# Performance work log

Measured on AMD Instinct MI355X. Metric: run time of the kernel, lower is better.

The kernel has to match this reference:

```python
import jax, jax.numpy as jnp
import numpy as np

N_NODES = 50000
N_EDGES = 800000
HID = 128
LAYERS = 3


def setup_inputs() -> dict:
    key = jax.random.key(0)
    k1, k2, k3, k4 = jax.random.split(key, 4)
    x = jax.random.normal(k1, (N_NODES, HID), dtype=jnp.float32)
    edge_index = jax.random.randint(k2, (2, N_EDGES), 0, N_NODES, dtype=jnp.int64)
    # Glorot-ish scale so 3 stacked layers stay numerically tame
    Ws = jax.random.normal(k3, (LAYERS, HID, HID), dtype=jnp.float32) * (1.0 / np.sqrt(HID))
    bs = jax.random.normal(k4, (LAYERS, HID), dtype=jnp.float32) * 0.01
    return {"x": x, "edge_index": edge_index, "Ws": Ws, "bs": bs}


def reference(x, edge_index, Ws, bs):
    """Stacked GCNConv (add_self_loops=False): out = D^-1/2 A D^-1/2 (x W) + b.
    Returns (final_x, embeddings_list) like the torch module."""
    N = x.shape[0]
    src = edge_index[0]  # message sources (x_j)
    dst = edge_index[1]  # aggregation targets
    # gcn_norm with unit edge weights, no self loops: in-degree on targets
    deg = jax.ops.segment_sum(jnp.ones(src.shape[0], dtype=x.dtype), dst, num_segments=N)
    dinv = jnp.where(deg > 0, jax.lax.rsqrt(jnp.maximum(deg, 1.0)), 0.0).astype(x.dtype)
    norm = dinv[src] * dinv[dst]  # [E]

    embeddings = [x]
    for l in range(Ws.shape[0]):
        h = x @ Ws[l]                               # [N, D] dense transform
        msg = h[src] * norm[:, None]                # [E, D] gather + normalize
        x = jax.ops.segment_sum(msg, dst, num_segments=N) + bs[l]  # scatter-add
        embeddings.append(x)
    return (x, embeddings)
```

## Files before the change

kernel.cpp:

```cpp
#include <hip/hip_runtime.h>

#define N_NODES 50000
#define N_EDGES 800000
#define HID 128
#define SLOT (N_NODES * HID)
#define W_STRIDE (HID * HID)

#define OFF_CNT    0ul
#define OFF_DINV   200192ul
#define OFF_RPTR   400384ul
#define OFF_RFILL  600576ul
#define OFF_BSUM   800768ul
#define OFF_BOFS   801280ul
#define OFF_SRCS   801792ul
#define OFF_H_WS   4001792ul


__global__ void k_zero_cnt(int* __restrict__ cnt) {
    int i = blockIdx.x * blockDim.x + threadIdx.x;
    if (i < N_NODES) cnt[i] = 0;
}

__global__ void k_count(const int* __restrict__ ei, int* __restrict__ cnt) {
    int e = blockIdx.x * blockDim.x + threadIdx.x;
    if (e < N_EDGES) {
        int d = ei[N_EDGES + e];
        atomicAdd(&cnt[d], 1);
    }
}

__global__ void k_dinv(const int* __restrict__ cnt, float* __restrict__ dinv) {
    int i = blockIdx.x * blockDim.x + threadIdx.x;
    if (i < N_NODES) {
        int c = cnt[i];
        dinv[i] = (c > 0) ? rsqrtf((float)c) : 0.0f;
    }
}

__global__ void k_scan_block(const int* __restrict__ cnt, int* __restrict__ rptr,
                             int* __restrict__ bsum) {
    __shared__ int s[512];
    int tid = threadIdx.x;
    int gid = blockIdx.x * 512 + tid;
    int v = (gid < N_NODES) ? cnt[gid] : 0;
    s[tid] = v;
    __syncthreads();
    for (int off = 1; off < 512; off <<= 1) {
        int t = (tid >= off) ? s[tid - off] : 0;
        __syncthreads();
        s[tid] += t;
        __syncthreads();
    }
    if (gid < N_NODES) rptr[gid] = s[tid] - v;
    if (tid == 511) bsum[blockIdx.x] = s[511];
}

__global__ void k_scan_sums(const int* __restrict__ bsum, int* __restrict__ bofs, int nb) {
    __shared__ int s[128];
    int tid = threadIdx.x;
    int v = (tid < nb) ? bsum[tid] : 0;
    s[tid] = v;
    __syncthreads();
    for (int off = 1; off < 128; off <<= 1) {
        int t = (tid >= off) ? s[tid - off] : 0;
        __syncthreads();
        s[tid] += t;
        __syncthreads();
    }
    if (tid < nb) bofs[tid] = s[tid] - v;
}

__global__ void k_scan_add(int* __restrict__ rptr, int* __restrict__ rfill,
                           const int* __restrict__ bofs) {
    int gid = blockIdx.x * blockDim.x + threadIdx.x;
    if (gid < N_NODES) {
        int r = rptr[gid] + bofs[gid >> 9];
        rptr[gid] = r;
        rfill[gid] = r;
    }
    if (gid == 0) rptr[N_NODES] = N_EDGES;
}

__global__ void k_scatter(const int* __restrict__ ei, int* __restrict__ rfill,
                          int* __restrict__ srcs) {
    int e = blockIdx.x * blockDim.x + threadIdx.x;
    if (e < N_EDGES) {
        int sv = ei[e];
        int d  = ei[N_EDGES + e];
        int pos = atomicAdd(&rfill[d], 1);
        srcs[pos] = sv;
    }
}

__launch_bounds__(256, 4)
__global__ void k_gemm_scale(const float* __restrict__ X, const float* __restrict__ W,
                             const float* __restrict__ dinv, float* __restrict__ H) {
    __shared__ float sX[64 * HID];
    int tid = threadIdx.x;
    int row0 = blockIdx.x * 64;

    const float4* X4  = (const float4*)X;
    float4*       sX4 = (float4*)sX;
    for (int j = tid; j < 2048; j += 256) {
        int r   = j >> 5;
        int c4  = j & 31;
        int row = row0 + r;
        float4 v = {0.f, 0.f, 0.f, 0.f};
        if (row < N_NODES) v = X4[row * 32 + c4];
        sX4[r * 32 + (c4 ^ ((r >> 3) & 7))] = v;
    }
    __syncthreads();

    int ty  = tid >> 4;
    int tx  = tid & 15;
    int swz = (ty >> 1) & 7;

    float4 acc[4][2];
    #pragma unroll
    for (int r = 0; r < 4; ++r) {
        acc[r][0] = {0.f, 0.f, 0.f, 0.f};
        acc[r][1] = {0.f, 0.f, 0.f, 0.f};
    }

    const float4* W4 = (const float4*)W;

    #pragma unroll 2
    for (int k0 = 0; k0 < HID; k0 += 4) {
        int k4 = k0 >> 2;
        float4 wv[4][2];
        #pragma unroll
        for (int kk = 0; kk < 4; ++kk) {
            wv[kk][0] = W4[(k0 + kk) * 32 + tx * 2 + 0];
            wv[kk][1] = W4[(k0 + kk) * 32 + tx * 2 + 1];
        }
        float4 xv[4];
        #pragma unroll
        for (int r = 0; r < 4; ++r)
            xv[r] = sX4[(ty * 4 + r) * 32 + (k4 ^ swz)];
        #pragma unroll
        for (int r = 0; r < 4; ++r) {
            float xk0 = xv[r].x, xk1 = xv[r].y, xk2 = xv[r].z, xk3 = xv[r].w;
            #pragma unroll
            for (int hh = 0; hh < 2; ++hh) {
                acc[r][hh].x += xk0 * wv[0][hh].x + xk1 * wv[1][hh].x + xk2 * wv[2][hh].x + xk3 * wv[3][hh].x;
                acc[r][hh].y += xk0 * wv[0][hh].y + xk1 * wv[1][hh].y + xk2 * wv[2][hh].y + xk3 * wv[3][hh].y;
                acc[r][hh].z += xk0 * wv[0][hh].z + xk1 * wv[1][hh].z + xk2 * wv[2][hh].z + xk3 * wv[3][hh].z;
                acc[r][hh].w += xk0 * wv[0][hh].w + xk1 * wv[1][hh].w + xk2 * wv[2][hh].w + xk3 * wv[3][hh].w;
            }
        }
    }

    float4* H4 = (float4*)H;
    #pragma unroll
    for (int r = 0; r < 4; ++r) {
        int row = row0 + ty * 4 + r;
        if (row < N_NODES) {
            float dv = dinv[row];
            float4 o0 = acc[r][0], o1 = acc[r][1];
            o0.x *= dv; o0.y *= dv; o0.z *= dv; o0.w *= dv;
            o1.x *= dv; o1.y *= dv; o1.z *= dv; o1.w *= dv;
            H4[row * 32 + tx * 2 + 0] = o0;
            H4[row * 32 + tx * 2 + 1] = o1;
        }
    }
}

__global__ void k_agg(const float* __restrict__ H, const int* __restrict__ rptr,
                      const int* __restrict__ srcs, const float* __restrict__ dinv,
                      const float* __restrict__ bias, float* __restrict__ out0,
                      float* __restrict__ out1) {
    int wid  = (blockIdx.x * blockDim.x + threadIdx.x) >> 6;
    int lane = threadIdx.x & 63;
    if (wid >= N_NODES) return;
    int half = lane >> 5;
    int l32  = lane & 31;

    int beg = rptr[wid];
    int end = rptr[wid + 1];
    int deg = end - beg;

    const float4* H4 = (const float4*)H;

    float4 a0 = {0.f,0.f,0.f,0.f}, a1 = {0.f,0.f,0.f,0.f};
    float4 a2 = {0.f,0.f,0.f,0.f}, a3 = {0.f,0.f,0.f,0.f};

    int p = beg;
    int n8 = beg + (deg & ~7);
    for (; p < n8; p += 8) {
        int base = p + half * 4;
        int s0 = srcs[base + 0];
        int s1 = srcs[base + 1];
        int s2 = srcs[base + 2];
        int s3 = srcs[base + 3];
        float4 h0 = H4[s0 * 32 + l32];
        float4 h1 = H4[s1 * 32 + l32];
        float4 h2 = H4[s2 * 32 + l32];
        float4 h3 = H4[s3 * 32 + l32];
        a0.x += h0.x; a0.y += h0.y; a0.z += h0.z; a0.w += h0.w;
        a1.x += h1.x; a1.y += h1.y; a1.z += h1.z; a1.w += h1.w;
        a2.x += h2.x; a2.y += h2.y; a2.z += h2.z; a2.w += h2.w;
        a3.x += h3.x; a3.y += h3.y; a3.z += h3.z; a3.w += h3.w;
    }
    int rem   = deg & 7;
    int pairs = rem >> 1;
    for (int i = 0; i < pairs; ++i) {
        int e = p + 2 * i + half;
        float4 hv = H4[srcs[e] * 32 + l32];
        if (i == 0)      { a0.x += hv.x; a0.y += hv.y; a0.z += hv.z; a0.w += hv.w; }
        else if (i == 1) { a1.x += hv.x; a1.y += hv.y; a1.z += hv.z; a1.w += hv.w; }
        else             { a2.x += hv.x; a2.y += hv.y; a2.z += hv.z; a2.w += hv.w; }
    }
    if (rem & 1) {
        float4 hv = H4[srcs[end - 1] * 32 + l32];
        if (half == 0) { a3.x += hv.x; a3.y += hv.y; a3.z += hv.z; a3.w += hv.w; }
    }

    float4 s;
    s.x = a0.x + a1.x + a2.x + a3.x;
    s.y = a0.y + a1.y + a2.y + a3.y;
    s.z = a0.z + a1.z + a2.z + a3.z;
    s.w = a0.w + a1.w + a2.w + a3.w;
    s.x += __shfl_xor(s.x, 32);
    s.y += __shfl_xor(s.y, 32);
    s.z += __shfl_xor(s.z, 32);
    s.w += __shfl_xor(s.w, 32);

    if (half == 0) {
        float dv  = dinv[wid];
        float4 bb = ((const float4*)bias)[l32];
        float4 res;
        res.x = s.x * dv + bb.x;
        res.y = s.y * dv + bb.y;
        res.z = s.z * dv + bb.z;
        res.w = s.w * dv + bb.w;
        ((float4*)out0)[wid * 32 + l32] = res;
        if (out1) ((float4*)out1)[wid * 32 + l32] = res;
    }
}

__global__ void k_copy(const float* __restrict__ src, float* __restrict__ dst, int n4) {
    int i = blockIdx.x * blockDim.x + threadIdx.x;
    if (i < n4) ((float4*)dst)[i] = ((const float4*)src)[i];
}


extern "C" void kernel_launch(void* const* d_in, const int* in_sizes, int n_in,
                              void* d_out, int out_size, void* d_ws, size_t ws_size,
                              hipStream_t stream) {
    const float* x  = (const float*)d_in[0];
    const int*   ei = (const int*)d_in[1];
    const float* Ws = (const float*)d_in[2];
    const float* bs = (const float*)d_in[3];
    float* out = (float*)d_out;
    char*  ws  = (char*)d_ws;

    int*   cnt   = (int*)  (ws + OFF_CNT);
    float* dinv  = (float*)(ws + OFF_DINV);
    int*   rptr  = (int*)  (ws + OFF_RPTR);
    int*   rfill = (int*)  (ws + OFF_RFILL);
    int*   bsum  = (int*)  (ws + OFF_BSUM);
    int*   bofs  = (int*)  (ws + OFF_BOFS);
    int*   srcs  = (int*)  (ws + OFF_SRCS);

    float* slot0 = out;
    float* slot1 = out + 1l * SLOT;
    float* slot2 = out + 2l * SLOT;
    float* slot3 = out + 3l * SLOT;
    float* slot4 = out + 4l * SLOT;

    bool   h_in_ws = ws_size >= (size_t)(OFF_H_WS + (size_t)SLOT * 4);
    float* h = h_in_ws ? (float*)(ws + OFF_H_WS) : slot0;

    const int NB_NODE = (N_NODES + 255) / 256;
    const int NB_EDGE = (N_EDGES + 255) / 256;
    const int NB_SCAN = (N_NODES + 511) / 512;

    k_zero_cnt  <<<NB_NODE, 256, 0, stream>>>(cnt);
    k_count     <<<NB_EDGE, 256, 0, stream>>>(ei, cnt);
    k_dinv      <<<NB_NODE, 256, 0, stream>>>(cnt, dinv);
    k_scan_block<<<NB_SCAN, 512, 0, stream>>>(cnt, rptr, bsum);
    k_scan_sums <<<1, 128, 0, stream>>>(bsum, bofs, NB_SCAN);
    k_scan_add  <<<NB_NODE, 256, 0, stream>>>(rptr, rfill, bofs);
    k_scatter   <<<NB_EDGE, 256, 0, stream>>>(ei, rfill, srcs);

    k_copy<<<SLOT / 4 / 256, 256, 0, stream>>>(x, slot1, SLOT / 4);

    const int NB_GEMM = (N_NODES + 63) / 64;
    const int NB_AGG  = (N_NODES + 3) / 4;

    k_gemm_scale<<<NB_GEMM, 256, 0, stream>>>(x, Ws + 0 * W_STRIDE, dinv, h);
    k_agg       <<<NB_AGG, 256, 0, stream>>>(h, rptr, srcs, dinv, bs + 0 * HID, slot2, nullptr);

    k_gemm_scale<<<NB_GEMM, 256, 0, stream>>>(slot2, Ws + 1 * W_STRIDE, dinv, h);
    k_agg       <<<NB_AGG, 256, 0, stream>>>(h, rptr, srcs, dinv, bs + 1 * HID, slot3, nullptr);

    k_gemm_scale<<<NB_GEMM, 256, 0, stream>>>(slot3, Ws + 2 * W_STRIDE, dinv, h);
    if (h_in_ws) {
        k_agg<<<NB_AGG, 256, 0, stream>>>(h, rptr, srcs, dinv, bs + 2 * HID, slot4, slot0);
    } else {
        k_agg<<<NB_AGG, 256, 0, stream>>>(h, rptr, srcs, dinv, bs + 2 * HID, slot4, nullptr);
        k_copy<<<SLOT / 4 / 256, 256, 0, stream>>>(slot4, slot0, SLOT / 4);
    }
}
```

Before: 415.8 us.

## Split GEMM output columns across blocks with W staged in LDS; fuse dinv into scan_add

```diff
diff --git a/kernel.cpp b/kernel.cpp
--- a/kernel.cpp
+++ b/kernel.cpp
@@ -26,14 +26,6 @@
     if (e < N_EDGES) {
         int d = ei[N_EDGES + e];
         atomicAdd(&cnt[d], 1);
-    }
-}
-
-__global__ void k_dinv(const int* __restrict__ cnt, float* __restrict__ dinv) {
-    int i = blockIdx.x * blockDim.x + threadIdx.x;
-    if (i < N_NODES) {
-        int c = cnt[i];
-        dinv[i] = (c > 0) ? rsqrtf((float)c) : 0.0f;
     }
 }
 
@@ -71,12 +63,15 @@
 }
 
 __global__ void k_scan_add(int* __restrict__ rptr, int* __restrict__ rfill,
-                           const int* __restrict__ bofs) {
+                           const int* __restrict__ bofs, const int* __restrict__ cnt,
+                           float* __restrict__ dinv) {
     int gid = blockIdx.x * blockDim.x + threadIdx.x;
     if (gid < N_NODES) {
         int r = rptr[gid] + bofs[gid >> 9];
         rptr[gid] = r;
         rfill[gid] = r;
+        int c = cnt[gid];
+        dinv[gid] = (c > 0) ? rsqrtf((float)c) : 0.0f;
     }
     if (gid == 0) rptr[N_NODES] = N_EDGES;
 }
@@ -92,12 +87,22 @@
     }
 }
 
-__launch_bounds__(256, 4)
+__launch_bounds__(256, 2)
 __global__ void k_gemm_scale(const float* __restrict__ X, const float* __restrict__ W,
                              const float* __restrict__ dinv, float* __restrict__ H) {
+    __shared__ float sW[HID * 64];
     __shared__ float sX[64 * HID];
-    int tid = threadIdx.x;
-    int row0 = blockIdx.x * 64;
+    int tid   = threadIdx.x;
+    int chalf = blockIdx.x & 1;
+    int row0  = (blockIdx.x >> 1) * 64;
+
+    const float4* W4  = (const float4*)W;
+    float4*       sW4 = (float4*)sW;
+    for (int j = tid; j < 2048; j += 256) {
+        int k  = j >> 4;
+        int c4 = j & 15;
+        sW4[j] = W4[k * 32 + chalf * 16 + c4];
+    }
 
     const float4* X4  = (const float4*)X;
     float4*       sX4 = (float4*)sX;
@@ -115,24 +120,17 @@
     int tx  = tid & 15;
     int swz = (ty >> 1) & 7;
 
-    float4 acc[4][2];
+    float4 acc[4];
     #pragma unroll
-    for (int r = 0; r < 4; ++r) {
-        acc[r][0] = {0.f, 0.f, 0.f, 0.f};
-        acc[r][1] = {0.f, 0.f, 0.f, 0.f};
-    }
-
-    const float4* W4 = (const float4*)W;
-
-    #pragma unroll 2
+    for (int r = 0; r < 4; ++r) acc[r] = {0.f, 0.f, 0.f, 0.f};
+
+    #pragma unroll 4
     for (int k0 = 0; k0 < HID; k0 += 4) {
         int k4 = k0 >> 2;
-        float4 wv[4][2];
+        float4 wv[4];
         #pragma unroll
-        for (int kk = 0; kk < 4; ++kk) {
-            wv[kk][0] = W4[(k0 + kk) * 32 + tx * 2 + 0];
-            wv[kk][1] = W4[(k0 + kk) * 32 + tx * 2 + 1];
-        }
+        for (int kk = 0; kk < 4; ++kk)
+            wv[kk] = sW4[(k0 + kk) * 16 + tx];
         float4 xv[4];
         #pragma unroll
         for (int r = 0; r < 4; ++r)
@@ -140,13 +138,10 @@
         #pragma unroll
         for (int r = 0; r < 4; ++r) {
             float xk0 = xv[r].x, xk1 = xv[r].y, xk2 = xv[r].z, xk3 = xv[r].w;
-            #pragma unroll
-            for (int hh = 0; hh < 2; ++hh) {
-                acc[r][hh].x += xk0 * wv[0][hh].x + xk1 * wv[1][hh].x + xk2 * wv[2][hh].x + xk3 * wv[3][hh].x;
-                acc[r][hh].y += xk0 * wv[0][hh].y + xk1 * wv[1][hh].y + xk2 * wv[2][hh].y + xk3 * wv[3][hh].y;
-                acc[r][hh].z += xk0 * wv[0][hh].z + xk1 * wv[1][hh].z + xk2 * wv[2][hh].z + xk3 * wv[3][hh].z;
-                acc[r][hh].w += xk0 * wv[0][hh].w + xk1 * wv[1][hh].w + xk2 * wv[2][hh].w + xk3 * wv[3][hh].w;
-            }
+            acc[r].x += xk0 * wv[0].x + xk1 * wv[1].x + xk2 * wv[2].x + xk3 * wv[3].x;
+            acc[r].y += xk0 * wv[0].y + xk1 * wv[1].y + xk2 * wv[2].y + xk3 * wv[3].y;
+            acc[r].z += xk0 * wv[0].z + xk1 * wv[1].z + xk2 * wv[2].z + xk3 * wv[3].z;
+            acc[r].w += xk0 * wv[0].w + xk1 * wv[1].w + xk2 * wv[2].w + xk3 * wv[3].w;
         }
     }
 
@@ -156,11 +151,9 @@
         int row = row0 + ty * 4 + r;
         if (row < N_NODES) {
             float dv = dinv[row];
-            float4 o0 = acc[r][0], o1 = acc[r][1];
-            o0.x *= dv; o0.y *= dv; o0.z *= dv; o0.w *= dv;
-            o1.x *= dv; o1.y *= dv; o1.z *= dv; o1.w *= dv;
-            H4[row * 32 + tx * 2 + 0] = o0;
-            H4[row * 32 + tx * 2 + 1] = o1;
+            float4 o = acc[r];
+            o.x *= dv; o.y *= dv; o.z *= dv; o.w *= dv;
+            H4[row * 32 + chalf * 16 + tx] = o;
         }
     }
 }
@@ -277,15 +270,14 @@
 
     k_zero_cnt  <<<NB_NODE, 256, 0, stream>>>(cnt);
     k_count     <<<NB_EDGE, 256, 0, stream>>>(ei, cnt);
-    k_dinv      <<<NB_NODE, 256, 0, stream>>>(cnt, dinv);
     k_scan_block<<<NB_SCAN, 512, 0, stream>>>(cnt, rptr, bsum);
     k_scan_sums <<<1, 128, 0, stream>>>(bsum, bofs, NB_SCAN);
-    k_scan_add  <<<NB_NODE, 256, 0, stream>>>(rptr, rfill, bofs);
+    k_scan_add  <<<NB_NODE, 256, 0, stream>>>(rptr, rfill, bofs, cnt, dinv);
     k_scatter   <<<NB_EDGE, 256, 0, stream>>>(ei, rfill, srcs);
 
     k_copy<<<SLOT / 4 / 256, 256, 0, stream>>>(x, slot1, SLOT / 4);
 
-    const int NB_GEMM = (N_NODES + 63) / 64;
+    const int NB_GEMM = 2 * ((N_NODES + 63) / 64);
     const int NB_AGG  = (N_NODES + 3) / 4;
 
     k_gemm_scale<<<NB_GEMM, 256, 0, stream>>>(x, Ws + 0 * W_STRIDE, dinv, h);
```

Measured after the change: 399.9 us. 1.04x faster.
